# Optimization experiments

Hardware: AMD Instinct MI355X
Metric: run time of the kernel (lower is better)

The kernel has to match this reference:

```python
import jax, jax.numpy as jnp
import numpy as np

MAX_DELTAS = 4  # number of concurrently loaded delta adapters


def _dequant(qw, qz, sc):
    """GPTQ-style 4-bit dequant with a single group (g_idx == 0).

    qw: [D, O, K//8] int32, 8 x 4-bit values packed along the input (K) dim.
    qz: [D, O//8, 1] int32, 8 x 4-bit zero points packed along the output dim.
    sc: [D, O, 1] float scales (one group).
    Returns dense delta weights [D, O, K].
    """
    shifts = jnp.arange(8, dtype=jnp.int32) * 4
    D, O, Kp = qw.shape
    w = ((qw[:, :, :, None] >> shifts) & 0xF).reshape(D, O, Kp * 8)   # [D,O,K]
    z = ((qz[:, :, 0][:, :, None] >> shifts) & 0xF).reshape(D, O)     # [D,O]
    return (w.astype(sc.dtype) - (z.astype(sc.dtype) + 1.0)[:, :, None]) * sc


def setup_inputs() -> dict:
    key = jax.random.key(0)
    ks = jax.random.split(key, 16)
    T, IN = 1024, 4096
    Q, KV = 4096, 1024  # 32 q-heads, 8 kv-heads, head_size 128
    OUT = Q + 2 * KV    # 6144
    D, PACK = MAX_DELTAS, 8
    IMAX = np.int32(2**31 - 1)
    return {
        "x": jax.random.normal(ks[0], (T, IN), dtype=jnp.float32),
        "w_base": jax.random.normal(ks[1], (OUT, IN), dtype=jnp.float32) * 0.02,
        "bias": jax.random.normal(ks[2], (OUT,), dtype=jnp.float32) * 0.02,
        "qweight_q": jax.random.randint(ks[3], (D, Q, IN // PACK), 0, IMAX, dtype=jnp.int32),
        "qweight_k": jax.random.randint(ks[4], (D, KV, IN // PACK), 0, IMAX, dtype=jnp.int32),
        "qweight_v": jax.random.randint(ks[5], (D, KV, IN // PACK), 0, IMAX, dtype=jnp.int32),
        "qzeros_q": jax.random.randint(ks[6], (D, Q // PACK, 1), 0, IMAX, dtype=jnp.int32),
        "qzeros_k": jax.random.randint(ks[7], (D, KV // PACK, 1), 0, IMAX, dtype=jnp.int32),
        "qzeros_v": jax.random.randint(ks[8], (D, KV // PACK, 1), 0, IMAX, dtype=jnp.int32),
        "scales_q": jax.random.uniform(ks[9], (D, Q, 1), dtype=jnp.float32) * 0.01,
        "scales_k": jax.random.uniform(ks[10], (D, KV, 1), dtype=jnp.float32) * 0.01,
        "scales_v": jax.random.uniform(ks[11], (D, KV, 1), dtype=jnp.float32) * 0.01,
        "indices": jax.random.randint(ks[12], (T,), 0, D, dtype=jnp.int32),
    }


def reference(x, w_base, bias, qweight_q, qweight_k, qweight_v,
              qzeros_q, qzeros_k, qzeros_v, scales_q, scales_k, scales_v,
              indices):
    # Base fused QKV projection.
    out = x @ w_base.T + bias  # [T, OUT]
    # Dequantize the three packed delta stacks and concatenate along out dim,
    # matching the (q, k, v) output_slices scatter of apply_delta.
    Wd = jnp.concatenate([
        _dequant(qweight_q, qzeros_q, scales_q),
        _dequant(qweight_k, qzeros_k, scales_k),
        _dequant(qweight_v, qzeros_v, scales_v),
    ], axis=1)  # [D, OUT, IN]
    # Per-token indexed delta matmul: token t uses adapter indices[t].
    for d in range(MAX_DELTAS):
        xm = jnp.where((indices == d)[:, None], x, 0.0)  # [T, IN]
        out = out + xm @ Wd[d].T
    return out
```

## Files before the change

kernel.cpp:

```cpp
#include <hip/hip_runtime.h>
#include <stdint.h>

#define T_TOK 1024
#define K_IN  4096
#define N_OUT 6144
#define N_Q   4096
#define N_KV  1024
#define N_D   4
#define KP    512

#define TM 128
#define TN 128
#define BK 64
#define KSPLIT 2
#define KHALF (K_IN / KSPLIT)
#define NSTEPS (KHALF / BK)
#define PM_MAX 1536
#define MT (PM_MAX/TM)
#define NT (N_OUT/TN)
#define NBLK (NT * MT * KSPLIT)

typedef __attribute__((ext_vector_type(8)))  short  short8;
typedef __attribute__((ext_vector_type(4)))  float  float4v;
typedef __attribute__((ext_vector_type(4)))  float  f32x4;
typedef __attribute__((ext_vector_type(4)))  uint   u32x4;

__device__ __forceinline__ ushort f2bf(float f) {
    uint32_t u = __float_as_uint(f);
    u = (u + 0x7FFFu + ((u >> 16) & 1u)) >> 16;
    return (ushort)u;
}
__device__ __forceinline__ uint pack2(ushort a, ushort b) {
    return (uint)a | ((uint)b << 16);
}

__global__ void build_perm_kernel(const int* __restrict__ indices,
                                  int* __restrict__ perm,
                                  int* __restrict__ pofs) {
    __shared__ int cnt[N_D], cur[N_D], ps[N_D + 1];
    int tid = threadIdx.x;
    if (tid < N_D) { cnt[tid] = 0; cur[tid] = 0; }
    __syncthreads();
    for (int t = tid; t < T_TOK; t += blockDim.x) atomicAdd(&cnt[indices[t]], 1);
    for (int p = tid; p < PM_MAX; p += blockDim.x) perm[p] = -1;
    __syncthreads();
    if (tid == 0) {
        int run = 0;
        for (int d = 0; d < N_D; d++) { ps[d] = run; run += ((cnt[d] + TM - 1) / TM) * TM; }
        ps[N_D] = run;
        for (int d = 0; d <= N_D; d++) pofs[d] = ps[d];
    }
    __syncthreads();
    for (int t = tid; t < T_TOK; t += blockDim.x) {
        int d = indices[t];
        int r = atomicAdd(&cur[d], 1);
        perm[ps[d] + r] = t;
    }
}

__global__ void dequant_wall_kernel(const float* __restrict__ w_base,
                                    const int* __restrict__ qw_q, const int* __restrict__ qw_k, const int* __restrict__ qw_v,
                                    const int* __restrict__ qz_q, const int* __restrict__ qz_k, const int* __restrict__ qz_v,
                                    const float* __restrict__ sc_q, const float* __restrict__ sc_k, const float* __restrict__ sc_v,
                                    ushort* __restrict__ wall) {
    int id  = blockIdx.x * blockDim.x + threadIdx.x;
    int kq  = id & (KP - 1);
    int o   = id >> 9;

    const int* qw; const int* qz; const float* sc; int r, Osec;
    if (o < N_Q)            { qw = qw_q; qz = qz_q; sc = sc_q; r = o;                Osec = N_Q;  }
    else if (o < N_Q + N_KV){ qw = qw_k; qz = qz_k; sc = sc_k; r = o - N_Q;          Osec = N_KV; }
    else                    { qw = qw_v; qz = qz_v; sc = sc_v; r = o - (N_Q + N_KV); Osec = N_KV; }

    const f32x4* wbp = (const f32x4*)(w_base + (size_t)o * K_IN + (size_t)kq * 8);
    f32x4 wb0 = __builtin_nontemporal_load(wbp);
    f32x4 wb1 = __builtin_nontemporal_load(wbp + 1);
    float wb[8] = {wb0.x, wb0.y, wb0.z, wb0.w, wb1.x, wb1.y, wb1.z, wb1.w};

#pragma unroll
    for (int d = 0; d < N_D; d++) {
        int   q  = __builtin_nontemporal_load(qw + ((size_t)d * Osec + r) * KP + kq);
        int   zq = qz[(size_t)d * (Osec / 8) + (r >> 3)];
        float s  = sc[(size_t)d * Osec + r];
        float zs = (float)(((zq >> ((r & 7) * 4)) & 0xF) + 1) * s;

        ushort res[8];
#pragma unroll
        for (int j = 0; j < 8; j++) {
            float v = wb[j] + (float)((q >> (4 * j)) & 0xF) * s - zs;
            res[j] = f2bf(v);
        }
        u32x4 packv;
        packv.x = pack2(res[0], res[1]); packv.y = pack2(res[2], res[3]);
        packv.z = pack2(res[4], res[5]); packv.w = pack2(res[6], res[7]);
        *(u32x4*)(wall + ((size_t)d * N_OUT + o) * K_IN + (size_t)kq * 8) = packv;
    }
}

__global__ void build_xp_kernel(const float* __restrict__ x,
                                const int* __restrict__ perm,
                                ushort* __restrict__ xp) {
    int pm = blockIdx.x;
    int c0 = blockIdx.y * 2048 + threadIdx.x * 8;
    int tok = perm[pm];
    ushort res[8];
    if (tok < 0) {
#pragma unroll
        for (int j = 0; j < 8; j++) res[j] = 0;
    } else {
        const f32x4* src = (const f32x4*)(x + (size_t)tok * K_IN + c0);
        f32x4 a = __builtin_nontemporal_load(src);
        f32x4 b = __builtin_nontemporal_load(src + 1);
        float v[8] = {a.x, a.y, a.z, a.w, b.x, b.y, b.z, b.w};
#pragma unroll
        for (int j = 0; j < 8; j++) res[j] = f2bf(v[j]);
    }
    u32x4 packv;
    packv.x = pack2(res[0], res[1]); packv.y = pack2(res[2], res[3]);
    packv.z = pack2(res[4], res[5]); packv.w = pack2(res[6], res[7]);
    *(u32x4*)(xp + (size_t)pm * K_IN + c0) = packv;
}

__global__ void init_out_kernel(const float* __restrict__ bias,
                                float* __restrict__ out) {
    int id = blockIdx.x * blockDim.x + threadIdx.x;
    int n4 = id & (N_OUT / 4 - 1);
    int t  = id / (N_OUT / 4);
    float4 b = *(const float4*)(bias + n4 * 4);
    *(float4*)(out + (size_t)t * N_OUT + n4 * 4) = b;
}

__global__ __launch_bounds__(256, 2) void gemm_kernel(
    const ushort* __restrict__ xp, const ushort* __restrict__ wall,
    const int* __restrict__ perm, const int* __restrict__ pofs,
    float* __restrict__ out) {

    __shared__ ushort As[2][TM * BK];
    __shared__ ushort Bs[2][TN * BK];

    int lin  = blockIdx.x;
    int low3 = lin & 7, rest = lin >> 3;
    int j    = rest % 24, bq = rest / 24;
    int bn   = bq * 8 + low3;
    int bm   = j % MT, kz = j / MT;

    int m0 = bm * TM, n0 = bn * TN;
    int ptot = pofs[N_D];
    if (m0 >= ptot) return;
    int d = 0;
    while (d < N_D - 1 && m0 >= pofs[d + 1]) d++;

    const ushort* wsec = wall + (size_t)d * N_OUT * K_IN;

    int tid  = threadIdx.x;
    int lane = tid & 63;
    int wv   = tid >> 6;
    int wm   = (wv & 1) * 64;
    int wn   = (wv >> 1) * 64;
    int quad = lane >> 4;
    int l16  = lane & 15;
    int xa   = l16 & 7;

    const float4v zero4 = {0.f, 0.f, 0.f, 0.f};
    float4v acc[4][4];
#pragma unroll
    for (int i = 0; i < 4; i++)
#pragma unroll
        for (int jj = 0; jj < 4; jj++) acc[i][jj] = zero4;

    auto stage = [&](ushort* dstA, ushort* dstB, int k0) {
#pragma unroll
        for (int w = 0; w < 4; w++) {
            int p   = w * 256 + tid;
            int row = p >> 3;
            int ckl = (p & 7) ^ (row & 7);
            const ushort* ga = xp   + (size_t)(m0 + row) * K_IN + k0 + ckl * 8;
            const ushort* gb = wsec + (size_t)(n0 + row) * K_IN + k0 + ckl * 8;
            int base = (w * 256 + (tid & ~63)) * 8;
            __builtin_amdgcn_global_load_lds((const __attribute__((address_space(1))) void*)ga,
                                             (__attribute__((address_space(3))) void*)(dstA + base), 16, 0, 0);
            __builtin_amdgcn_global_load_lds((const __attribute__((address_space(1))) void*)gb,
                                             (__attribute__((address_space(3))) void*)(dstB + base), 16, 0, 0);
        }
    };

    int kbase = kz * KHALF;
    int buf = 0;
    stage(As[0], Bs[0], kbase);
    __syncthreads();

    for (int s = 0; s < NSTEPS; s++) {
        if (s + 1 < NSTEPS) stage(As[1 - buf], Bs[1 - buf], kbase + (s + 1) * BK);

        const ushort* Ab = As[buf];
        const ushort* Bb = Bs[buf];
#pragma unroll
        for (int kk = 0; kk < BK; kk += 32) {
            int ckb = (kk >> 3) + quad;
            short8 a[4], b[4];
#pragma unroll
            for (int i = 0; i < 4; i++)
                a[i] = *(const short8*)(Ab + (wm + i * 16 + l16) * BK + (ckb ^ xa) * 8);
#pragma unroll
            for (int jj = 0; jj < 4; jj++)
                b[jj] = *(const short8*)(Bb + (wn + jj * 16 + l16) * BK + (ckb ^ xa) * 8);
#pragma unroll
            for (int i = 0; i < 4; i++)
#pragma unroll
                for (int jj = 0; jj < 4; jj++)
                    acc[i][jj] = __builtin_amdgcn_mfma_f32_16x16x32_bf16(a[i], b[jj], acc[i][jj], 0, 0, 0);
        }
        __syncthreads();
        buf ^= 1;
    }

#pragma unroll
    for (int i = 0; i < 4; i++) {
        int toks[4];
#pragma unroll
        for (int r = 0; r < 4; r++) toks[r] = perm[m0 + wm + i * 16 + quad * 4 + r];
#pragma unroll
        for (int jj = 0; jj < 4; jj++) {
            int col = n0 + wn + jj * 16 + l16;
#pragma unroll
            for (int r = 0; r < 4; r++) {
                int tok = toks[r];
                if (tok >= 0) atomicAdd(out + (size_t)tok * N_OUT + col, acc[i][jj][r]);
            }
        }
    }
}

extern "C" void kernel_launch(void* const* d_in, const int* in_sizes, int n_in,
                              void* d_out, int out_size, void* d_ws, size_t ws_size,
                              hipStream_t stream) {
    const float* x      = (const float*)d_in[0];
    const float* w_base = (const float*)d_in[1];
    const float* bias   = (const float*)d_in[2];
    const int*   qw_q   = (const int*)d_in[3];
    const int*   qw_k   = (const int*)d_in[4];
    const int*   qw_v   = (const int*)d_in[5];
    const int*   qz_q   = (const int*)d_in[6];
    const int*   qz_k   = (const int*)d_in[7];
    const int*   qz_v   = (const int*)d_in[8];
    const float* sc_q   = (const float*)d_in[9];
    const float* sc_k   = (const float*)d_in[10];
    const float* sc_v   = (const float*)d_in[11];
    const int*   indices= (const int*)d_in[12];
    float* out = (float*)d_out;

    char* ws = (char*)d_ws;
    ushort* wall = (ushort*)ws;
    size_t wall_bytes = (size_t)N_D * N_OUT * K_IN * 2;
    ushort* xp = (ushort*)(ws + wall_bytes);
    size_t xp_bytes = (size_t)PM_MAX * K_IN * 2;
    int* perm = (int*)(ws + wall_bytes + xp_bytes);
    int* pofs = perm + PM_MAX;

    build_perm_kernel<<<1, 256, 0, stream>>>(indices, perm, pofs);
    dequant_wall_kernel<<<(N_OUT * KP) / 256, 256, 0, stream>>>(
        w_base, qw_q, qw_k, qw_v, qz_q, qz_k, qz_v, sc_q, sc_k, sc_v, wall);
    build_xp_kernel<<<dim3(PM_MAX, 2), 256, 0, stream>>>(x, perm, xp);
    init_out_kernel<<<(T_TOK * N_OUT / 4) / 256, 256, 0, stream>>>(bias, out);
    gemm_kernel<<<NBLK, 256, 0, stream>>>(xp, wall, perm, pofs, out);
}
```

Before: 367.1 us.

## Fuse 4-bit delta dequant into GEMM via bf16 nibble trick and row-sum correction

Drops the pre-pass that materialised four dense bf16 merged weight copies. The GEMM now streams a single bf16 copy of the base weight. Packed 4-bit delta values are unpacked in registers into bf16 (128+n, built with the 0x4300 exponent trick) and fed to a second set of MFMAs. Scale and zero-point are applied algebraically in the epilogue, using per-row activation sums computed in build_xp. This removes the large weight-materialisation traffic but doubles the MFMA count and accumulator registers, which may hurt occupancy.

```diff
diff --git a/kernel.cpp b/kernel.cpp
--- a/kernel.cpp
+++ b/kernel.cpp
@@ -34,6 +34,16 @@
     return (uint)a | ((uint)b << 16);
 }
 
+__device__ __forceinline__ short8 unpack_nib(uint q) {
+    union { u32x4 u; short8 s; } r;
+    uint t1 = q >> 8, t2 = q >> 16, t3 = q >> 24;
+    r.u.x = ((q  & 0xFu) | ((q  & 0xF0u) << 12)) | 0x43004300u;
+    r.u.y = ((t1 & 0xFu) | ((t1 & 0xF0u) << 12)) | 0x43004300u;
+    r.u.z = ((t2 & 0xFu) | ((t2 & 0xF0u) << 12)) | 0x43004300u;
+    r.u.w = ((t3 & 0xFu) | ((t3 & 0xF0u) << 12)) | 0x43004300u;
+    return r.s;
+}
+
 __global__ void build_perm_kernel(const int* __restrict__ indices,
                                   int* __restrict__ perm,
                                   int* __restrict__ pofs) {
@@ -58,50 +68,27 @@
     }
 }
 
-__global__ void dequant_wall_kernel(const float* __restrict__ w_base,
-                                    const int* __restrict__ qw_q, const int* __restrict__ qw_k, const int* __restrict__ qw_v,
-                                    const int* __restrict__ qz_q, const int* __restrict__ qz_k, const int* __restrict__ qz_v,
-                                    const float* __restrict__ sc_q, const float* __restrict__ sc_k, const float* __restrict__ sc_v,
-                                    ushort* __restrict__ wall) {
-    int id  = blockIdx.x * blockDim.x + threadIdx.x;
-    int kq  = id & (KP - 1);
-    int o   = id >> 9;
-
-    const int* qw; const int* qz; const float* sc; int r, Osec;
-    if (o < N_Q)            { qw = qw_q; qz = qz_q; sc = sc_q; r = o;                Osec = N_Q;  }
-    else if (o < N_Q + N_KV){ qw = qw_k; qz = qz_k; sc = sc_k; r = o - N_Q;          Osec = N_KV; }
-    else                    { qw = qw_v; qz = qz_v; sc = sc_v; r = o - (N_Q + N_KV); Osec = N_KV; }
-
-    const f32x4* wbp = (const f32x4*)(w_base + (size_t)o * K_IN + (size_t)kq * 8);
-    f32x4 wb0 = __builtin_nontemporal_load(wbp);
-    f32x4 wb1 = __builtin_nontemporal_load(wbp + 1);
-    float wb[8] = {wb0.x, wb0.y, wb0.z, wb0.w, wb1.x, wb1.y, wb1.z, wb1.w};
-
-#pragma unroll
-    for (int d = 0; d < N_D; d++) {
-        int   q  = __builtin_nontemporal_load(qw + ((size_t)d * Osec + r) * KP + kq);
-        int   zq = qz[(size_t)d * (Osec / 8) + (r >> 3)];
-        float s  = sc[(size_t)d * Osec + r];
-        float zs = (float)(((zq >> ((r & 7) * 4)) & 0xF) + 1) * s;
-
-        ushort res[8];
-#pragma unroll
-        for (int j = 0; j < 8; j++) {
-            float v = wb[j] + (float)((q >> (4 * j)) & 0xF) * s - zs;
-            res[j] = f2bf(v);
-        }
-        u32x4 packv;
-        packv.x = pack2(res[0], res[1]); packv.y = pack2(res[2], res[3]);
-        packv.z = pack2(res[4], res[5]); packv.w = pack2(res[6], res[7]);
-        *(u32x4*)(wall + ((size_t)d * N_OUT + o) * K_IN + (size_t)kq * 8) = packv;
-    }
+__global__ void wbconv_kernel(const float* __restrict__ w_base,
+                              ushort* __restrict__ wb16) {
+    int id = blockIdx.x * blockDim.x + threadIdx.x;
+    const f32x4* src = (const f32x4*)(w_base + (size_t)id * 8);
+    f32x4 a = __builtin_nontemporal_load(src);
+    f32x4 b = __builtin_nontemporal_load(src + 1);
+    u32x4 packv;
+    packv.x = pack2(f2bf(a.x), f2bf(a.y));
+    packv.y = pack2(f2bf(a.z), f2bf(a.w));
+    packv.z = pack2(f2bf(b.x), f2bf(b.y));
+    packv.w = pack2(f2bf(b.z), f2bf(b.w));
+    *(u32x4*)(wb16 + (size_t)id * 8) = packv;
 }
 
 __global__ void build_xp_kernel(const float* __restrict__ x,
                                 const int* __restrict__ perm,
-                                ushort* __restrict__ xp) {
+                                ushort* __restrict__ xp,
+                                float* __restrict__ rs) {
     int pm = blockIdx.x;
-    int c0 = blockIdx.y * 2048 + threadIdx.x * 8;
+    int half = blockIdx.y;
+    int c0 = half * KHALF + threadIdx.x * 8;
     int tok = perm[pm];
     ushort res[8];
     if (tok < 0) {
@@ -119,6 +106,16 @@
     packv.x = pack2(res[0], res[1]); packv.y = pack2(res[2], res[3]);
     packv.z = pack2(res[4], res[5]); packv.w = pack2(res[6], res[7]);
     *(u32x4*)(xp + (size_t)pm * K_IN + c0) = packv;
+
+    float ssum = 0.f;
+#pragma unroll
+    for (int j = 0; j < 8; j++) ssum += __uint_as_float((uint)res[j] << 16);
+#pragma unroll
+    for (int off = 32; off > 0; off >>= 1) ssum += __shfl_xor(ssum, off);
+    __shared__ float wsum[4];
+    if ((threadIdx.x & 63) == 0) wsum[threadIdx.x >> 6] = ssum;
+    __syncthreads();
+    if (threadIdx.x == 0) rs[pm * 2 + half] = wsum[0] + wsum[1] + wsum[2] + wsum[3];
 }
 
 __global__ void init_out_kernel(const float* __restrict__ bias,
@@ -131,8 +128,12 @@
 }
 
 __global__ __launch_bounds__(256, 2) void gemm_kernel(
-    const ushort* __restrict__ xp, const ushort* __restrict__ wall,
+    const ushort* __restrict__ xp, const ushort* __restrict__ wb16,
+    const int* __restrict__ qw_q, const int* __restrict__ qw_k, const int* __restrict__ qw_v,
+    const int* __restrict__ qz_q, const int* __restrict__ qz_k, const int* __restrict__ qz_v,
+    const float* __restrict__ sc_q, const float* __restrict__ sc_k, const float* __restrict__ sc_v,
     const int* __restrict__ perm, const int* __restrict__ pofs,
+    const float* __restrict__ rs,
     float* __restrict__ out) {
 
     __shared__ ushort As[2][TM * BK];
@@ -150,7 +151,10 @@
     int d = 0;
     while (d < N_D - 1 && m0 >= pofs[d + 1]) d++;
 
-    const ushort* wsec = wall + (size_t)d * N_OUT * K_IN;
+    const int* qw; const int* qz; const float* sc; int r0, Osec;
+    if (n0 < N_Q)            { qw = qw_q; qz = qz_q; sc = sc_q; r0 = n0;                Osec = N_Q;  }
+    else if (n0 < N_Q + N_KV){ qw = qw_k; qz = qz_k; sc = sc_k; r0 = n0 - N_Q;          Osec = N_KV; }
+    else                     { qw = qw_v; qz = qz_v; sc = sc_v; r0 = n0 - (N_Q + N_KV); Osec = N_KV; }
 
     int tid  = threadIdx.x;
     int lane = tid & 63;
@@ -161,12 +165,20 @@
     int l16  = lane & 15;
     int xa   = l16 & 7;
 
+    int    rsec[4];
+    size_t qrow[4];
+#pragma unroll
+    for (int jj = 0; jj < 4; jj++) {
+        rsec[jj] = r0 + wn + jj * 16 + l16;
+        qrow[jj] = ((size_t)d * Osec + rsec[jj]) * KP;
+    }
+
     const float4v zero4 = {0.f, 0.f, 0.f, 0.f};
-    float4v acc[4][4];
+    float4v acc_b[4][4], acc_d[4][4];
 #pragma unroll
     for (int i = 0; i < 4; i++)
 #pragma unroll
-        for (int jj = 0; jj < 4; jj++) acc[i][jj] = zero4;
+        for (int jj = 0; jj < 4; jj++) { acc_b[i][jj] = zero4; acc_d[i][jj] = zero4; }
 
     auto stage = [&](ushort* dstA, ushort* dstB, int k0) {
 #pragma unroll
@@ -175,7 +187,7 @@
             int row = p >> 3;
             int ckl = (p & 7) ^ (row & 7);
             const ushort* ga = xp   + (size_t)(m0 + row) * K_IN + k0 + ckl * 8;
-            const ushort* gb = wsec + (size_t)(n0 + row) * K_IN + k0 + ckl * 8;
+            const ushort* gb = wb16 + (size_t)(n0 + row) * K_IN + k0 + ckl * 8;
             int base = (w * 256 + (tid & ~63)) * 8;
             __builtin_amdgcn_global_load_lds((const __attribute__((address_space(1))) void*)ga,
                                              (__attribute__((address_space(3))) void*)(dstA + base), 16, 0, 0);
@@ -187,17 +199,36 @@
     int kbase = kz * KHALF;
     int buf = 0;
     stage(As[0], Bs[0], kbase);
+
+    int q_cur[4][2], q_nxt[4][2];
+    {
+        int qo = kbase >> 3;
+#pragma unroll
+        for (int jj = 0; jj < 4; jj++)
+#pragma unroll
+            for (int h = 0; h < 2; h++)
+                q_cur[jj][h] = qw[qrow[jj] + qo + h * 4 + quad];
+    }
     __syncthreads();
 
     for (int s = 0; s < NSTEPS; s++) {
-        if (s + 1 < NSTEPS) stage(As[1 - buf], Bs[1 - buf], kbase + (s + 1) * BK);
+        if (s + 1 < NSTEPS) {
+            stage(As[1 - buf], Bs[1 - buf], kbase + (s + 1) * BK);
+            int qo = (kbase + (s + 1) * BK) >> 3;
+#pragma unroll
+            for (int jj = 0; jj < 4; jj++)
+#pragma unroll
+                for (int h = 0; h < 2; h++)
+                    q_nxt[jj][h] = qw[qrow[jj] + qo + h * 4 + quad];
+        }
 
         const ushort* Ab = As[buf];
         const ushort* Bb = Bs[buf];
 #pragma unroll
         for (int kk = 0; kk < BK; kk += 32) {
+            int h   = kk >> 5;
             int ckb = (kk >> 3) + quad;
-            short8 a[4], b[4];
+            short8 a[4], b[4], bd[4];
 #pragma unroll
             for (int i = 0; i < 4; i++)
                 a[i] = *(const short8*)(Ab + (wm + i * 16 + l16) * BK + (ckb ^ xa) * 8);
@@ -205,27 +236,53 @@
             for (int jj = 0; jj < 4; jj++)
                 b[jj] = *(const short8*)(Bb + (wn + jj * 16 + l16) * BK + (ckb ^ xa) * 8);
 #pragma unroll
+            for (int jj = 0; jj < 4; jj++)
+                bd[jj] = unpack_nib((uint)q_cur[jj][h]);
+#pragma unroll
             for (int i = 0; i < 4; i++)
 #pragma unroll
-                for (int jj = 0; jj < 4; jj++)
-                    acc[i][jj] = __builtin_amdgcn_mfma_f32_16x16x32_bf16(a[i], b[jj], acc[i][jj], 0, 0, 0);
+                for (int jj = 0; jj < 4; jj++) {
+                    acc_b[i][jj] = __builtin_amdgcn_mfma_f32_16x16x32_bf16(a[i], b[jj],  acc_b[i][jj], 0, 0, 0);
+                    acc_d[i][jj] = __builtin_amdgcn_mfma_f32_16x16x32_bf16(a[i], bd[jj], acc_d[i][jj], 0, 0, 0);
+                }
         }
         __syncthreads();
+#pragma unroll
+        for (int jj = 0; jj < 4; jj++)
+#pragma unroll
+            for (int h = 0; h < 2; h++)
+                q_cur[jj][h] = q_nxt[jj][h];
         buf ^= 1;
     }
 
+    float s4[4], cc4[4];
+#pragma unroll
+    for (int jj = 0; jj < 4; jj++) {
+        float sv = sc[(size_t)d * Osec + rsec[jj]];
+        int   zq = qz[(size_t)d * (Osec >> 3) + (rsec[jj] >> 3)];
+        int   z  = (zq >> ((rsec[jj] & 7) * 4)) & 0xF;
+        s4[jj]  = sv;
+        cc4[jj] = sv * (float)(129 + z);
+    }
 #pragma unroll
     for (int i = 0; i < 4; i++) {
-        int toks[4];
-#pragma unroll
-        for (int r = 0; r < 4; r++) toks[r] = perm[m0 + wm + i * 16 + quad * 4 + r];
+        int toks[4]; float rsv[4];
+#pragma unroll
+        for (int r = 0; r < 4; r++) {
+            int row = m0 + wm + i * 16 + quad * 4 + r;
+            toks[r] = perm[row];
+            rsv[r]  = rs[row * 2 + kz];
+        }
 #pragma unroll
         for (int jj = 0; jj < 4; jj++) {
             int col = n0 + wn + jj * 16 + l16;
 #pragma unroll
             for (int r = 0; r < 4; r++) {
                 int tok = toks[r];
-                if (tok >= 0) atomicAdd(out + (size_t)tok * N_OUT + col, acc[i][jj][r]);
+                if (tok >= 0) {
+                    float v = acc_b[i][jj][r] + s4[jj] * acc_d[i][jj][r] - cc4[jj] * rsv[r];
+                    atomicAdd(out + (size_t)tok * N_OUT + col, v);
+                }
             }
         }
     }
@@ -250,17 +307,20 @@
     float* out = (float*)d_out;
 
     char* ws = (char*)d_ws;
-    ushort* wall = (ushort*)ws;
-    size_t wall_bytes = (size_t)N_D * N_OUT * K_IN * 2;
-    ushort* xp = (ushort*)(ws + wall_bytes);
+    ushort* wb16 = (ushort*)ws;
+    size_t wb_bytes = (size_t)N_OUT * K_IN * 2;
+    ushort* xp = (ushort*)(ws + wb_bytes);
     size_t xp_bytes = (size_t)PM_MAX * K_IN * 2;
-    int* perm = (int*)(ws + wall_bytes + xp_bytes);
+    float* rsum = (float*)(ws + wb_bytes + xp_bytes);
+    size_t rs_bytes = (size_t)PM_MAX * KSPLIT * sizeof(float);
+    int* perm = (int*)(ws + wb_bytes + xp_bytes + rs_bytes);
     int* pofs = perm + PM_MAX;
 
     build_perm_kernel<<<1, 256, 0, stream>>>(indices, perm, pofs);
-    dequant_wall_kernel<<<(N_OUT * KP) / 256, 256, 0, stream>>>(
-        w_base, qw_q, qw_k, qw_v, qz_q, qz_k, qz_v, sc_q, sc_k, sc_v, wall);
-    build_xp_kernel<<<dim3(PM_MAX, 2), 256, 0, stream>>>(x, perm, xp);
+    wbconv_kernel<<<(N_OUT * K_IN / 8) / 256, 256, 0, stream>>>(w_base, wb16);
+    build_xp_kernel<<<dim3(PM_MAX, 2), 256, 0, stream>>>(x, perm, xp, rsum);
     init_out_kernel<<<(T_TOK * N_OUT / 4) / 256, 256, 0, stream>>>(bias, out);
-    gemm_kernel<<<NBLK, 256, 0, stream>>>(xp, wall, perm, pofs, out);
-}
+    gemm_kernel<<<NBLK, 256, 0, stream>>>(xp, wb16,
+        qw_q, qw_k, qw_v, qz_q, qz_k, qz_v, sc_q, sc_k, sc_v,
+        perm, pofs, rsum, out);
+}
```

Result: slower. 516.6 us (+40.7%).
